# Optimization experiments

Hardware: AMD Instinct MI355X
Metric: run time of the kernel (lower is better)

Reference implementation:

```python
import jax, jax.numpy as jnp
import numpy as np

B, S_VIT, S_Q, L = 64, 257, 32, 512
IMG, HID, C = 1408, 768, 30000
H_CLUB, H_MINE = 32, 64


def setup_inputs() -> dict:
    key = jax.random.key(0)
    ks = jax.random.split(key, 20)
    s = 0.02
    inp = {
        "vit": jax.random.normal(ks[0], (B, S_VIT, IMG), jnp.float32),
        "qformer": jax.random.normal(ks[1], (B, S_Q, HID), jnp.float32),
        "label_pre": jax.random.randint(ks[2], (B, L), 0, C, jnp.int32),
        "perm_idx": jax.random.permutation(ks[3], B).astype(jnp.int32),
        "rand_idx": jax.random.randint(ks[4], (B,), 0, B, jnp.int32),
        # CLUB params
        "W_mu1": jax.random.normal(ks[5], (HID, H_CLUB), jnp.float32) * s,
        "b_mu1": jnp.zeros((H_CLUB,), jnp.float32),
        "W_mu2": jax.random.normal(ks[6], (H_CLUB, C), jnp.float32) * s,
        "b_mu2": jnp.zeros((C,), jnp.float32),
        "W_lv1": jax.random.normal(ks[7], (HID, H_CLUB), jnp.float32) * s,
        "b_lv1": jnp.zeros((H_CLUB,), jnp.float32),
        "W_lv2": jax.random.normal(ks[8], (H_CLUB, C), jnp.float32) * s,
        "b_lv2": jnp.zeros((C,), jnp.float32),
        # MINE params
        "W_t1": jax.random.normal(ks[9], (IMG + HID, H_MINE), jnp.float32) * s,
        "b_t1": jnp.zeros((H_MINE,), jnp.float32),
        "W_t2": jax.random.normal(ks[10], (H_MINE, 1), jnp.float32) * s,
        "b_t2": jnp.zeros((1,), jnp.float32),
    }
    return inp


def reference(vit, qformer, label_pre, perm_idx, rand_idx,
              W_mu1, b_mu1, W_mu2, b_mu2, W_lv1, b_lv1, W_lv2, b_lv2,
              W_t1, b_t1, W_t2, b_t2):
    # label histogram == one_hot(label, C).mean(dim=1), computed via scatter-add
    label = jnp.where(label_pre == -100, 0, label_pre)  # (B, L)
    flat = (label + jnp.arange(B, dtype=label.dtype)[:, None] * C).ravel()
    y_hist = (jnp.zeros((B * C,), jnp.float32).at[flat].add(1.0)
              .reshape(B, C) / jnp.float32(L))  # (B, C)

    xq = qformer.mean(axis=1)  # (B, HID)

    # CLUBSample.forward(xq, y_hist)
    mu = jax.nn.relu(xq @ W_mu1 + b_mu1) @ W_mu2 + b_mu2          # (B, C)
    logvar = jnp.tanh(jax.nn.relu(xq @ W_lv1 + b_lv1) @ W_lv2 + b_lv2)
    inv_var = 1.0 / (jnp.exp(logvar) + 1e-6)
    pos = -(mu - y_hist) ** 2 * inv_var
    neg = -(mu - y_hist[perm_idx]) ** 2 * inv_var
    I_zy = (pos.sum(axis=-1) - neg.sum(axis=-1)).mean() / 2.0

    # MINE.forward(xv, xq)
    xv = vit.mean(axis=1)  # (B, IMG)

    def T(a, b):
        h = jnp.concatenate([a, b], axis=-1)
        return (jax.nn.relu(h @ W_t1 + b_t1) @ W_t2 + b_t2)[:, 0]

    T0 = T(xv, xq)
    T1 = T(xv, xq[rand_idx])
    I_xz = T0.mean() - (jax.nn.logsumexp(T1) - jnp.log(jnp.float32(B)))

    return I_zy - 0.1 * I_xz
```

## Files before the change

kernel.cpp:

```cpp
#include <hip/hip_runtime.h>
#include <hip/hip_bf16.h>
#include <math.h>

#define B       64
#define S_VIT   257
#define S_Q     32
#define L       512
#define IMG     1408
#define HID     768
#define C       30000
#define H_CLUB  32
#define H_MINE  64

#define OFF_XVSUM   0
#define OFF_YHIST   (OFF_XVSUM + B * IMG)
#define OFF_DV64    (OFF_YHIST + B * C)
#define OFF_DQ64    (OFF_DV64 + 2 * B * H_MINE)
#define WS_ZERO_FLOATS (OFF_DQ64 + 2 * B * H_MINE)
#define OFF_XQ      WS_ZERO_FLOATS
#define OFF_HMU     (OFF_XQ + B * HID)
#define OFF_HLV     (OFF_HMU + B * H_CLUB)
#define OFF_CLUBP   (OFF_HLV + B * H_CLUB)
#define N_CLUB_BLK_X 118
#define N_CLUB_BLK_Y 4
#define N_CLUB_PART (N_CLUB_BLK_X * N_CLUB_BLK_Y)

__global__ void k_stage_a(const float* __restrict__ vit, const float* __restrict__ qf,
                          const int* __restrict__ label,
                          float* __restrict__ xv_sum, float* __restrict__ xq,
                          float* __restrict__ y_hist) {
    const int blk = blockIdx.x;
    const int tid = threadIdx.x;
    if (blk < 512) {
        const int b     = blk >> 3;
        const int split = blk & 7;
        const int s0 = split * 33;
        const int s1 = (s0 + 33 < S_VIT) ? s0 + 33 : S_VIT;
        const float4* row = (const float4*)(vit + (size_t)b * S_VIT * IMG);
        float4 a0 = make_float4(0.f, 0.f, 0.f, 0.f);
        float4 a1 = make_float4(0.f, 0.f, 0.f, 0.f);
        const bool second = (tid < 96);
        for (int s = s0; s < s1; ++s) {
            const float4* p = row + (size_t)s * (IMG / 4);
            float4 v = p[tid];
            a0.x += v.x; a0.y += v.y; a0.z += v.z; a0.w += v.w;
            if (second) {
                float4 w = p[tid + 256];
                a1.x += w.x; a1.y += w.y; a1.z += w.z; a1.w += w.w;
            }
        }
        float* out = xv_sum + (size_t)b * IMG;
        atomicAdd(&out[tid * 4 + 0], a0.x);
        atomicAdd(&out[tid * 4 + 1], a0.y);
        atomicAdd(&out[tid * 4 + 2], a0.z);
        atomicAdd(&out[tid * 4 + 3], a0.w);
        if (second) {
            atomicAdd(&out[(tid + 256) * 4 + 0], a1.x);
            atomicAdd(&out[(tid + 256) * 4 + 1], a1.y);
            atomicAdd(&out[(tid + 256) * 4 + 2], a1.z);
            atomicAdd(&out[(tid + 256) * 4 + 3], a1.w);
        }
    } else if (blk < 560) {
        const int idx = (blk - 512) * 256 + tid;
        const int b  = idx / (HID / 4);
        const int k4 = idx % (HID / 4);
        const float* base = qf + (size_t)b * S_Q * HID + k4 * 4;
        float4 s = make_float4(0.f, 0.f, 0.f, 0.f);
        #pragma unroll
        for (int t = 0; t < S_Q; ++t) {
            const float4 v = *(const float4*)(base + (size_t)t * HID);
            s.x += v.x; s.y += v.y; s.z += v.z; s.w += v.w;
        }
        const float inv = 1.0f / (float)S_Q;
        s.x *= inv; s.y *= inv; s.z *= inv; s.w *= inv;
        ((float4*)xq)[(size_t)b * (HID / 4) + k4] = s;
    } else {
        const int idx = (blk - 560) * 256 + tid;
        for (int t = idx; t < B * L; t += 2048) {
            int lab = label[t];
            if (lab == -100) lab = 0;
            const int b = t >> 9;
            atomicAdd(&y_hist[(size_t)b * C + lab], 1.0f);
        }
    }
}

__global__ void __launch_bounds__(256, 2)
k_stage_b(const float* __restrict__ xv_sum, const float* __restrict__ xq,
          const float* __restrict__ W_t1,
          const float* __restrict__ W_mu1, const float* __restrict__ b_mu1,
          const float* __restrict__ W_lv1, const float* __restrict__ b_lv1,
          double* __restrict__ dv, double* __restrict__ dq,
          float* __restrict__ h_mu, float* __restrict__ h_lv) {
    const int blk = blockIdx.x;
    const int tid = threadIdx.x;
    if (blk < 256) {
        __shared__ double s_v[4][H_MINE];
        __shared__ double s_q[4][H_MINE];
        const int b  = blk >> 2;
        const int q  = blk & 3;
        const int j  = tid & 63;
        const int kk = tid >> 6;
        const float* xvb = xv_sum + (size_t)b * IMG;
        const float* xqb = xq + (size_t)b * HID;

        double a0 = 0, a1 = 0, a2 = 0, a3 = 0;
        {
            const int k0 = q * (IMG / 4) + kk * (IMG / 16);
            #pragma unroll 2
            for (int t = 0; t < IMG / 16; t += 4) {
                const int k = k0 + t;
                a0 = fma((double)xvb[k],     (double)W_t1[(size_t)(k)     * H_MINE + j], a0);
                a1 = fma((double)xvb[k + 1], (double)W_t1[(size_t)(k + 1) * H_MINE + j], a1);
                a2 = fma((double)xvb[k + 2], (double)W_t1[(size_t)(k + 2) * H_MINE + j], a2);
                a3 = fma((double)xvb[k + 3], (double)W_t1[(size_t)(k + 3) * H_MINE + j], a3);
            }
        }
        s_v[kk][j] = (a0 + a1) + (a2 + a3);

        double q0 = 0, q1 = 0, q2 = 0, q3 = 0;
        {
            const int k0 = q * (HID / 4) + kk * (HID / 16);
            #pragma unroll 2
            for (int t = 0; t < HID / 16; t += 4) {
                const int k = k0 + t;
                q0 = fma((double)xqb[k],     (double)W_t1[(size_t)(IMG + k)     * H_MINE + j], q0);
                q1 = fma((double)xqb[k + 1], (double)W_t1[(size_t)(IMG + k + 1) * H_MINE + j], q1);
                q2 = fma((double)xqb[k + 2], (double)W_t1[(size_t)(IMG + k + 2) * H_MINE + j], q2);
                q3 = fma((double)xqb[k + 3], (double)W_t1[(size_t)(IMG + k + 3) * H_MINE + j], q3);
            }
        }
        s_q[kk][j] = (q0 + q1) + (q2 + q3);
        __syncthreads();
        if (tid < H_MINE) {
            double sv = (s_v[0][tid] + s_v[1][tid]) + (s_v[2][tid] + s_v[3][tid]);
            double sq = (s_q[0][tid] + s_q[1][tid]) + (s_q[2][tid] + s_q[3][tid]);
            atomicAdd(&dv[b * H_MINE + tid], sv * (1.0 / (double)S_VIT));
            atomicAdd(&dq[b * H_MINE + tid], sq);
        }
    } else {
        __shared__ float  sx[HID];
        __shared__ double s_mu[32][H_CLUB];
        __shared__ double s_lv[32][H_CLUB];
        const int b = blk - 256;
        for (int i = tid; i < HID; i += 256) sx[i] = xq[(size_t)b * HID + i];
        __syncthreads();
        const int h4 = (tid & 7) * 4;
        const int kk = tid >> 3;
        const int k0 = kk * 24;
        double m0 = 0, m1 = 0, m2 = 0, m3 = 0;
        double l0 = 0, l1 = 0, l2 = 0, l3 = 0;
        #pragma unroll 4
        for (int t = 0; t < 24; ++t) {
            const int k = k0 + t;
            const float4 wm = *(const float4*)&W_mu1[(size_t)k * H_CLUB + h4];
            const float4 wl = *(const float4*)&W_lv1[(size_t)k * H_CLUB + h4];
            const double xv = (double)sx[k];
            m0 = fma(xv, (double)wm.x, m0);
            m1 = fma(xv, (double)wm.y, m1);
            m2 = fma(xv, (double)wm.z, m2);
            m3 = fma(xv, (double)wm.w, m3);
            l0 = fma(xv, (double)wl.x, l0);
            l1 = fma(xv, (double)wl.y, l1);
            l2 = fma(xv, (double)wl.z, l2);
            l3 = fma(xv, (double)wl.w, l3);
        }
        s_mu[kk][h4 + 0] = m0; s_mu[kk][h4 + 1] = m1;
        s_mu[kk][h4 + 2] = m2; s_mu[kk][h4 + 3] = m3;
        s_lv[kk][h4 + 0] = l0; s_lv[kk][h4 + 1] = l1;
        s_lv[kk][h4 + 2] = l2; s_lv[kk][h4 + 3] = l3;
        __syncthreads();
        if (tid < H_CLUB) {
            double am = (double)b_mu1[tid], al = (double)b_lv1[tid];
            #pragma unroll
            for (int i = 0; i < 32; ++i) { am += s_mu[i][tid]; al += s_lv[i][tid]; }
            h_mu[b * H_CLUB + tid] = fmaxf((float)am, 0.f);
            h_lv[b * H_CLUB + tid] = fmaxf((float)al, 0.f);
        }
    }
}

__global__ void k_club_main(const float* __restrict__ W_mu2, const float* __restrict__ b_mu2,
                            const float* __restrict__ W_lv2, const float* __restrict__ b_lv2,
                            const float* __restrict__ h_mu, const float* __restrict__ h_lv,
                            const float* __restrict__ y_hist, const int* __restrict__ perm,
                            double* __restrict__ club_partial) {
    __shared__ float s_hmu[16 * H_CLUB];
    __shared__ float s_hlv[16 * H_CLUB];
    __shared__ int   s_perm[16];
    __shared__ double red[256];
    const int tid = threadIdx.x;
    const int c   = blockIdx.x * 256 + tid;
    const int b0  = blockIdx.y * 16;
    if (tid < 16) s_perm[tid] = perm[b0 + tid];
    for (int i = tid; i < 16 * H_CLUB; i += 256) {
        s_hmu[i] = h_mu[b0 * H_CLUB + i];
        s_hlv[i] = h_lv[b0 * H_CLUB + i];
    }
    __syncthreads();

    double total = 0.0;
    if (c < C) {
        float wm[H_CLUB], wl[H_CLUB];
        #pragma unroll
        for (int h = 0; h < H_CLUB; ++h) {
            wm[h] = W_mu2[(size_t)h * C + c];
            wl[h] = W_lv2[(size_t)h * C + c];
        }
        const float bm = b_mu2[c], bl = b_lv2[c];
        for (int bb = 0; bb < 16; ++bb) {
            float mu = bm, lv = bl;
            #pragma unroll
            for (int h = 0; h < H_CLUB; ++h) {
                mu = fmaf(s_hmu[bb * H_CLUB + h], wm[h], mu);
                lv = fmaf(s_hlv[bb * H_CLUB + h], wl[h], lv);
            }
            const float th = tanhf(lv);
            const float iv = 1.0f / (expf(th) + 1e-6f);
            const int b = b0 + bb;
            const float y  = y_hist[(size_t)b * C + c] * (1.0f / (float)L);
            const float yp = y_hist[(size_t)s_perm[bb] * C + c] * (1.0f / (float)L);
            const float dn = mu - yp;
            const float dp = mu - y;
            total += (double)(iv * (dn * dn - dp * dp));
        }
    }
    red[tid] = total;
    __syncthreads();
    for (int off = 128; off > 0; off >>= 1) {
        if (tid < off) red[tid] += red[tid + off];
        __syncthreads();
    }
    if (tid == 0) club_partial[blockIdx.y * gridDim.x + blockIdx.x] = red[0];
}

__global__ void k_final(const double* __restrict__ dv, const double* __restrict__ dq,
                        const float* __restrict__ b_t1, const float* __restrict__ W_t2,
                        const float* __restrict__ b_t2, const int* __restrict__ rand_idx,
                        const double* __restrict__ club_partial,
                        float* __restrict__ out) {
    __shared__ double red[256];
    const int tid = threadIdx.x;
    double cp = 0.0;
    for (int i = tid; i < N_CLUB_PART; i += 256) cp += club_partial[i];
    red[tid] = cp;
    __syncthreads();
    for (int off = 128; off > 0; off >>= 1) {
        if (tid < off) red[tid] += red[tid + off];
        __syncthreads();
    }
    const double club_total = red[0];

    if (tid < B) {
        const int b  = tid;
        const int rb = rand_idx[b];
        double a0 = 0.0, a1 = 0.0;
        #pragma unroll 4
        for (int j = 0; j < H_MINE; ++j) {
            const double base_v = dv[b * H_MINE + j] + (double)b_t1[j];
            const double v0 = base_v + dq[b * H_MINE + j];
            const double v1 = base_v + dq[rb * H_MINE + j];
            const double w = (double)W_t2[j];
            a0 = fma(fmax(v0, 0.0), w, a0);
            a1 = fma(fmax(v1, 0.0), w, a1);
        }
        const double T0 = a0 + (double)b_t2[0];
        const double T1 = a1 + (double)b_t2[0];

        double msum = T0;
        #pragma unroll
        for (int off = 32; off > 0; off >>= 1) msum += __shfl_down(msum, off, 64);
        double mx = T1;
        #pragma unroll
        for (int off = 32; off > 0; off >>= 1) mx = fmax(mx, __shfl_down(mx, off, 64));
        mx = __shfl(mx, 0, 64);
        double e = exp(T1 - mx);
        #pragma unroll
        for (int off = 32; off > 0; off >>= 1) e += __shfl_down(e, off, 64);

        if (tid == 0) {
            const double mean0 = msum * (1.0 / (double)B);
            const double lse   = mx + log(e);
            const double I_xz  = mean0 - (lse - log((double)B));
            const double I_zy  = club_total / (2.0 * (double)B);
            out[0] = (float)(I_zy - 0.1 * I_xz);
        }
    }
}

extern "C" void kernel_launch(void* const* d_in, const int* in_sizes, int n_in,
                              void* d_out, int out_size, void* d_ws, size_t ws_size,
                              hipStream_t stream) {
    const float* vit     = (const float*)d_in[0];
    const float* qformer = (const float*)d_in[1];
    const int*   label   = (const int*)d_in[2];
    const int*   perm    = (const int*)d_in[3];
    const int*   randi   = (const int*)d_in[4];
    const float* W_mu1   = (const float*)d_in[5];
    const float* b_mu1   = (const float*)d_in[6];
    const float* W_mu2   = (const float*)d_in[7];
    const float* b_mu2   = (const float*)d_in[8];
    const float* W_lv1   = (const float*)d_in[9];
    const float* b_lv1   = (const float*)d_in[10];
    const float* W_lv2   = (const float*)d_in[11];
    const float* b_lv2   = (const float*)d_in[12];
    const float* W_t1    = (const float*)d_in[13];
    const float* b_t1    = (const float*)d_in[14];
    const float* W_t2    = (const float*)d_in[15];
    const float* b_t2    = (const float*)d_in[16];

    float* ws      = (float*)d_ws;
    float* xv_sum  = ws + OFF_XVSUM;
    float* y_hist  = ws + OFF_YHIST;
    double* dv64   = (double*)(ws + OFF_DV64);
    double* dq64   = (double*)(ws + OFF_DQ64);
    float* xq      = ws + OFF_XQ;
    float* h_mu    = ws + OFF_HMU;
    float* h_lv    = ws + OFF_HLV;
    double* club_p = (double*)(ws + OFF_CLUBP);

    hipMemsetAsync(ws, 0, (size_t)WS_ZERO_FLOATS * sizeof(float), stream);

    k_stage_a<<<568, 256, 0, stream>>>(vit, qformer, label, xv_sum, xq, y_hist);
    k_stage_b<<<320, 256, 0, stream>>>(xv_sum, xq, W_t1, W_mu1, b_mu1, W_lv1, b_lv1,
                                       dv64, dq64, h_mu, h_lv);
    k_club_main<<<dim3(N_CLUB_BLK_X, N_CLUB_BLK_Y), 256, 0, stream>>>(
        W_mu2, b_mu2, W_lv2, b_lv2, h_mu, h_lv, y_hist, perm, club_p);
    k_final<<<1, 256, 0, stream>>>(dv64, dq64, b_t1, W_t2, b_t2, randi, club_p, (float*)d_out);
}
```

Baseline: 220.9 us.

## Fuse final reduction into CLUB kernel via last-block atomic ticket

Merges the single-block final kernel into the CLUB main kernel. Each block writes its partial, takes an atomic ticket on a zeroed counter, and the last block to finish does the cross-block reduction plus the MINE tail. The CLUB inner loop also reads the hidden vectors from shared memory as float4 instead of scalar loads. This removes one kernel launch and its gap at the cost of extra fences and an atomic per block.

Result: slower. 228.8 us (+3.6%).

```diff
diff --git a/kernel.cpp b/kernel.cpp
--- a/kernel.cpp
+++ b/kernel.cpp
@@ -16,7 +16,8 @@
 #define OFF_YHIST   (OFF_XVSUM + B * IMG)
 #define OFF_DV64    (OFF_YHIST + B * C)
 #define OFF_DQ64    (OFF_DV64 + 2 * B * H_MINE)
-#define WS_ZERO_FLOATS (OFF_DQ64 + 2 * B * H_MINE)
+#define OFF_CTR     (OFF_DQ64 + 2 * B * H_MINE)
+#define WS_ZERO_FLOATS (OFF_CTR + 4)
 #define OFF_XQ      WS_ZERO_FLOATS
 #define OFF_HMU     (OFF_XQ + B * HID)
 #define OFF_HLV     (OFF_HMU + B * H_CLUB)
@@ -180,15 +181,21 @@
     }
 }
 
-__global__ void k_club_main(const float* __restrict__ W_mu2, const float* __restrict__ b_mu2,
-                            const float* __restrict__ W_lv2, const float* __restrict__ b_lv2,
-                            const float* __restrict__ h_mu, const float* __restrict__ h_lv,
-                            const float* __restrict__ y_hist, const int* __restrict__ perm,
-                            double* __restrict__ club_partial) {
-    __shared__ float s_hmu[16 * H_CLUB];
-    __shared__ float s_hlv[16 * H_CLUB];
+__global__ void k_club_final(const float* __restrict__ W_mu2, const float* __restrict__ b_mu2,
+                             const float* __restrict__ W_lv2, const float* __restrict__ b_lv2,
+                             const float* __restrict__ h_mu, const float* __restrict__ h_lv,
+                             const float* __restrict__ y_hist, const int* __restrict__ perm,
+                             double* __restrict__ club_partial,
+                             const double* __restrict__ dv, const double* __restrict__ dq,
+                             const float* __restrict__ b_t1, const float* __restrict__ W_t2,
+                             const float* __restrict__ b_t2, const int* __restrict__ rand_idx,
+                             unsigned int* __restrict__ ctr,
+                             float* __restrict__ out) {
+    __shared__ __align__(16) float s_hmu[16 * H_CLUB];
+    __shared__ __align__(16) float s_hlv[16 * H_CLUB];
     __shared__ int   s_perm[16];
     __shared__ double red[256];
+    __shared__ unsigned int s_ticket;
     const int tid = threadIdx.x;
     const int c   = blockIdx.x * 256 + tid;
     const int b0  = blockIdx.y * 16;
@@ -209,11 +216,22 @@
         }
         const float bm = b_mu2[c], bl = b_lv2[c];
         for (int bb = 0; bb < 16; ++bb) {
+            const float4* hm4 = (const float4*)&s_hmu[bb * H_CLUB];
+            const float4* hl4 = (const float4*)&s_hlv[bb * H_CLUB];
             float mu = bm, lv = bl;
             #pragma unroll
-            for (int h = 0; h < H_CLUB; ++h) {
-                mu = fmaf(s_hmu[bb * H_CLUB + h], wm[h], mu);
-                lv = fmaf(s_hlv[bb * H_CLUB + h], wl[h], lv);
+            for (int h8 = 0; h8 < 8; ++h8) {
+                const float4 hm = hm4[h8];
+                const float4 hl = hl4[h8];
+                const int h = h8 * 4;
+                mu = fmaf(hm.x, wm[h + 0], mu);
+                mu = fmaf(hm.y, wm[h + 1], mu);
+                mu = fmaf(hm.z, wm[h + 2], mu);
+                mu = fmaf(hm.w, wm[h + 3], mu);
+                lv = fmaf(hl.x, wl[h + 0], lv);
+                lv = fmaf(hl.y, wl[h + 1], lv);
+                lv = fmaf(hl.z, wl[h + 2], lv);
+                lv = fmaf(hl.w, wl[h + 3], lv);
             }
             const float th = tanhf(lv);
             const float iv = 1.0f / (expf(th) + 1e-6f);
@@ -231,16 +249,15 @@
         if (tid < off) red[tid] += red[tid + off];
         __syncthreads();
     }
-    if (tid == 0) club_partial[blockIdx.y * gridDim.x + blockIdx.x] = red[0];
-}
-
-__global__ void k_final(const double* __restrict__ dv, const double* __restrict__ dq,
-                        const float* __restrict__ b_t1, const float* __restrict__ W_t2,
-                        const float* __restrict__ b_t2, const int* __restrict__ rand_idx,
-                        const double* __restrict__ club_partial,
-                        float* __restrict__ out) {
-    __shared__ double red[256];
-    const int tid = threadIdx.x;
+    if (tid == 0) {
+        club_partial[blockIdx.y * gridDim.x + blockIdx.x] = red[0];
+        __threadfence();
+        s_ticket = atomicAdd(ctr, 1u);
+    }
+    __syncthreads();
+    if (s_ticket != N_CLUB_PART - 1) return;
+    __threadfence();
+
     double cp = 0.0;
     for (int i = tid; i < N_CLUB_PART; i += 256) cp += club_partial[i];
     red[tid] = cp;
@@ -314,6 +331,7 @@
     float* y_hist  = ws + OFF_YHIST;
     double* dv64   = (double*)(ws + OFF_DV64);
     double* dq64   = (double*)(ws + OFF_DQ64);
+    unsigned int* ctr = (unsigned int*)(ws + OFF_CTR);
     float* xq      = ws + OFF_XQ;
     float* h_mu    = ws + OFF_HMU;
     float* h_lv    = ws + OFF_HLV;
@@ -324,7 +342,7 @@
     k_stage_a<<<568, 256, 0, stream>>>(vit, qformer, label, xv_sum, xq, y_hist);
     k_stage_b<<<320, 256, 0, stream>>>(xv_sum, xq, W_t1, W_mu1, b_mu1, W_lv1, b_lv1,
                                        dv64, dq64, h_mu, h_lv);
-    k_club_main<<<dim3(N_CLUB_BLK_X, N_CLUB_BLK_Y), 256, 0, stream>>>(
-        W_mu2, b_mu2, W_lv2, b_lv2, h_mu, h_lv, y_hist, perm, club_p);
-    k_final<<<1, 256, 0, stream>>>(dv64, dq64, b_t1, W_t2, b_t2, randi, club_p, (float*)d_out);
+    k_club_final<<<dim3(N_CLUB_BLK_X, N_CLUB_BLK_Y), 256, 0, stream>>>(
+        W_mu2, b_mu2, W_lv2, b_lv2, h_mu, h_lv, y_hist, perm, club_p,
+        dv64, dq64, b_t1, W_t2, b_t2, randi, ctr, (float*)d_out);
 }
```

## Skip CLUB classes absent from labels and fuse stages with last-block reduction

Applied to the files above, without the earlier changes.

The term (mu-yp)^2-(mu-y)^2 is zero for any class that appears in neither sample b's labels nor its permuted partner's labels. So each batch block now builds a shared-memory hash set of those labels and evaluates mu and logvar only for that sparse set, instead of all 30000 classes for every batch. The CLUB first layer, the sparse CLUB evaluation, the MINE projection and the final reduction are fused into one kernel. A global atomic ticket lets the last block finish the reduction, which removes two launches and the h_mu/h_lv round-trip. The vit mean is also split across 16 blocks per batch instead of 8. The cost is scattered strided reads of W_mu2/W_lv2 columns, hash insertion contention, and larger shared-memory usage per block.

Result: slower. 312.1 us (+41.2%).

```diff
diff --git a/kernel.cpp b/kernel.cpp
--- a/kernel.cpp
+++ b/kernel.cpp
@@ -16,14 +16,12 @@
 #define OFF_YHIST   (OFF_XVSUM + B * IMG)
 #define OFF_DV64    (OFF_YHIST + B * C)
 #define OFF_DQ64    (OFF_DV64 + 2 * B * H_MINE)
-#define WS_ZERO_FLOATS (OFF_DQ64 + 2 * B * H_MINE)
+#define OFF_CTR     (OFF_DQ64 + 2 * B * H_MINE)
+#define WS_ZERO_FLOATS (OFF_CTR + 4)
 #define OFF_XQ      WS_ZERO_FLOATS
-#define OFF_HMU     (OFF_XQ + B * HID)
-#define OFF_HLV     (OFF_HMU + B * H_CLUB)
-#define OFF_CLUBP   (OFF_HLV + B * H_CLUB)
-#define N_CLUB_BLK_X 118
-#define N_CLUB_BLK_Y 4
-#define N_CLUB_PART (N_CLUB_BLK_X * N_CLUB_BLK_Y)
+#define OFF_CLUBP   (OFF_XQ + B * HID)
+
+#define N_BC_BLOCKS (256 + B)
 
 __global__ void k_stage_a(const float* __restrict__ vit, const float* __restrict__ qf,
                           const int* __restrict__ label,
@@ -31,11 +29,11 @@
                           float* __restrict__ y_hist) {
     const int blk = blockIdx.x;
     const int tid = threadIdx.x;
-    if (blk < 512) {
-        const int b     = blk >> 3;
-        const int split = blk & 7;
-        const int s0 = split * 33;
-        const int s1 = (s0 + 33 < S_VIT) ? s0 + 33 : S_VIT;
+    if (blk < 1024) {
+        const int b     = blk >> 4;
+        const int split = blk & 15;
+        const int s0 = (split * S_VIT) >> 4;
+        const int s1 = ((split + 1) * S_VIT) >> 4;
         const float4* row = (const float4*)(vit + (size_t)b * S_VIT * IMG);
         float4 a0 = make_float4(0.f, 0.f, 0.f, 0.f);
         float4 a1 = make_float4(0.f, 0.f, 0.f, 0.f);
@@ -60,8 +58,8 @@
             atomicAdd(&out[(tid + 256) * 4 + 2], a1.z);
             atomicAdd(&out[(tid + 256) * 4 + 3], a1.w);
         }
-    } else if (blk < 560) {
-        const int idx = (blk - 512) * 256 + tid;
+    } else if (blk < 1072) {
+        const int idx = (blk - 1024) * 256 + tid;
         const int b  = idx / (HID / 4);
         const int k4 = idx % (HID / 4);
         const float* base = qf + (size_t)b * S_Q * HID + k4 * 4;
@@ -75,7 +73,7 @@
         s.x *= inv; s.y *= inv; s.z *= inv; s.w *= inv;
         ((float4*)xq)[(size_t)b * (HID / 4) + k4] = s;
     } else {
-        const int idx = (blk - 560) * 256 + tid;
+        const int idx = (blk - 1072) * 256 + tid;
         for (int t = idx; t < B * L; t += 2048) {
             int lab = label[t];
             if (lab == -100) lab = 0;
@@ -86,17 +84,36 @@
 }
 
 __global__ void __launch_bounds__(256, 2)
-k_stage_b(const float* __restrict__ xv_sum, const float* __restrict__ xq,
-          const float* __restrict__ W_t1,
-          const float* __restrict__ W_mu1, const float* __restrict__ b_mu1,
-          const float* __restrict__ W_lv1, const float* __restrict__ b_lv1,
-          double* __restrict__ dv, double* __restrict__ dq,
-          float* __restrict__ h_mu, float* __restrict__ h_lv) {
+k_stage_bc(const float* __restrict__ xv_sum, const float* __restrict__ xq,
+           const float* __restrict__ W_t1,
+           const float* __restrict__ W_mu1, const float* __restrict__ b_mu1,
+           const float* __restrict__ W_lv1, const float* __restrict__ b_lv1,
+           const float* __restrict__ W_mu2, const float* __restrict__ b_mu2,
+           const float* __restrict__ W_lv2, const float* __restrict__ b_lv2,
+           const float* __restrict__ y_hist, const int* __restrict__ label,
+           const int* __restrict__ perm, const int* __restrict__ rand_idx,
+           const float* __restrict__ b_t1, const float* __restrict__ W_t2,
+           const float* __restrict__ b_t2,
+           double* __restrict__ dv, double* __restrict__ dq,
+           double* __restrict__ club_partial, unsigned int* __restrict__ ctr,
+           float* __restrict__ out) {
+    __shared__ double s_v[4][H_MINE];
+    __shared__ double s_q[4][H_MINE];
+    __shared__ float  sx[HID];
+    __shared__ double s_mu[32][H_CLUB];
+    __shared__ double s_lv[32][H_CLUB];
+    __shared__ float  s_hmu[H_CLUB];
+    __shared__ float  s_hlv[H_CLUB];
+    __shared__ int    htab[2048];
+    __shared__ int    s_list[1024];
+    __shared__ int    s_nlist;
+    __shared__ double red[256];
+    __shared__ unsigned int s_ticket;
+
     const int blk = blockIdx.x;
     const int tid = threadIdx.x;
+
     if (blk < 256) {
-        __shared__ double s_v[4][H_MINE];
-        __shared__ double s_q[4][H_MINE];
         const int b  = blk >> 2;
         const int q  = blk & 3;
         const int j  = tid & 63;
@@ -139,110 +156,102 @@
             atomicAdd(&dq[b * H_MINE + tid], sq);
         }
     } else {
-        __shared__ float  sx[HID];
-        __shared__ double s_mu[32][H_CLUB];
-        __shared__ double s_lv[32][H_CLUB];
-        const int b = blk - 256;
+        const int b  = blk - 256;
+        const int pb = perm[b];
         for (int i = tid; i < HID; i += 256) sx[i] = xq[(size_t)b * HID + i];
         __syncthreads();
-        const int h4 = (tid & 7) * 4;
-        const int kk = tid >> 3;
-        const int k0 = kk * 24;
-        double m0 = 0, m1 = 0, m2 = 0, m3 = 0;
-        double l0 = 0, l1 = 0, l2 = 0, l3 = 0;
-        #pragma unroll 4
-        for (int t = 0; t < 24; ++t) {
-            const int k = k0 + t;
-            const float4 wm = *(const float4*)&W_mu1[(size_t)k * H_CLUB + h4];
-            const float4 wl = *(const float4*)&W_lv1[(size_t)k * H_CLUB + h4];
-            const double xv = (double)sx[k];
-            m0 = fma(xv, (double)wm.x, m0);
-            m1 = fma(xv, (double)wm.y, m1);
-            m2 = fma(xv, (double)wm.z, m2);
-            m3 = fma(xv, (double)wm.w, m3);
-            l0 = fma(xv, (double)wl.x, l0);
-            l1 = fma(xv, (double)wl.y, l1);
-            l2 = fma(xv, (double)wl.z, l2);
-            l3 = fma(xv, (double)wl.w, l3);
-        }
-        s_mu[kk][h4 + 0] = m0; s_mu[kk][h4 + 1] = m1;
-        s_mu[kk][h4 + 2] = m2; s_mu[kk][h4 + 3] = m3;
-        s_lv[kk][h4 + 0] = l0; s_lv[kk][h4 + 1] = l1;
-        s_lv[kk][h4 + 2] = l2; s_lv[kk][h4 + 3] = l3;
+        {
+            const int h4 = (tid & 7) * 4;
+            const int kk = tid >> 3;
+            const int k0 = kk * 24;
+            double m0 = 0, m1 = 0, m2 = 0, m3 = 0;
+            double l0 = 0, l1 = 0, l2 = 0, l3 = 0;
+            #pragma unroll 4
+            for (int t = 0; t < 24; ++t) {
+                const int k = k0 + t;
+                const float4 wm = *(const float4*)&W_mu1[(size_t)k * H_CLUB + h4];
+                const float4 wl = *(const float4*)&W_lv1[(size_t)k * H_CLUB + h4];
+                const double xv = (double)sx[k];
+                m0 = fma(xv, (double)wm.x, m0);
+                m1 = fma(xv, (double)wm.y, m1);
+                m2 = fma(xv, (double)wm.z, m2);
+                m3 = fma(xv, (double)wm.w, m3);
+                l0 = fma(xv, (double)wl.x, l0);
+                l1 = fma(xv, (double)wl.y, l1);
+                l2 = fma(xv, (double)wl.z, l2);
+                l3 = fma(xv, (double)wl.w, l3);
+            }
+            s_mu[kk][h4 + 0] = m0; s_mu[kk][h4 + 1] = m1;
+            s_mu[kk][h4 + 2] = m2; s_mu[kk][h4 + 3] = m3;
+            s_lv[kk][h4 + 0] = l0; s_lv[kk][h4 + 1] = l1;
+            s_lv[kk][h4 + 2] = l2; s_lv[kk][h4 + 3] = l3;
+        }
+        for (int i = tid; i < 2048; i += 256) htab[i] = -1;
+        if (tid == 0) s_nlist = 0;
         __syncthreads();
         if (tid < H_CLUB) {
             double am = (double)b_mu1[tid], al = (double)b_lv1[tid];
             #pragma unroll
             for (int i = 0; i < 32; ++i) { am += s_mu[i][tid]; al += s_lv[i][tid]; }
-            h_mu[b * H_CLUB + tid] = fmaxf((float)am, 0.f);
-            h_lv[b * H_CLUB + tid] = fmaxf((float)al, 0.f);
-        }
-    }
-}
-
-__global__ void k_club_main(const float* __restrict__ W_mu2, const float* __restrict__ b_mu2,
-                            const float* __restrict__ W_lv2, const float* __restrict__ b_lv2,
-                            const float* __restrict__ h_mu, const float* __restrict__ h_lv,
-                            const float* __restrict__ y_hist, const int* __restrict__ perm,
-                            double* __restrict__ club_partial) {
-    __shared__ float s_hmu[16 * H_CLUB];
-    __shared__ float s_hlv[16 * H_CLUB];
-    __shared__ int   s_perm[16];
-    __shared__ double red[256];
-    const int tid = threadIdx.x;
-    const int c   = blockIdx.x * 256 + tid;
-    const int b0  = blockIdx.y * 16;
-    if (tid < 16) s_perm[tid] = perm[b0 + tid];
-    for (int i = tid; i < 16 * H_CLUB; i += 256) {
-        s_hmu[i] = h_mu[b0 * H_CLUB + i];
-        s_hlv[i] = h_lv[b0 * H_CLUB + i];
-    }
-    __syncthreads();
-
-    double total = 0.0;
-    if (c < C) {
-        float wm[H_CLUB], wl[H_CLUB];
-        #pragma unroll
-        for (int h = 0; h < H_CLUB; ++h) {
-            wm[h] = W_mu2[(size_t)h * C + c];
-            wl[h] = W_lv2[(size_t)h * C + c];
-        }
-        const float bm = b_mu2[c], bl = b_lv2[c];
-        for (int bb = 0; bb < 16; ++bb) {
-            float mu = bm, lv = bl;
+            s_hmu[tid] = fmaxf((float)am, 0.f);
+            s_hlv[tid] = fmaxf((float)al, 0.f);
+        }
+        for (int i = tid; i < 2 * L; i += 256) {
+            int raw = (i < L) ? label[(size_t)b * L + i] : label[(size_t)pb * L + (i - L)];
+            int c = (raw == -100) ? 0 : raw;
+            int slot = c & 2047;
+            while (true) {
+                int prev = atomicCAS(&htab[slot], -1, c);
+                if (prev == -1) { int p = atomicAdd(&s_nlist, 1); s_list[p] = c; break; }
+                if (prev == c) break;
+                slot = (slot + 1) & 2047;
+            }
+        }
+        __syncthreads();
+        const int nl = s_nlist;
+        double total = 0.0;
+        for (int i = tid; i < nl; i += 256) {
+            const int c = s_list[i];
+            float wm[H_CLUB], wl[H_CLUB];
             #pragma unroll
             for (int h = 0; h < H_CLUB; ++h) {
-                mu = fmaf(s_hmu[bb * H_CLUB + h], wm[h], mu);
-                lv = fmaf(s_hlv[bb * H_CLUB + h], wl[h], lv);
+                wm[h] = W_mu2[(size_t)h * C + c];
+                wl[h] = W_lv2[(size_t)h * C + c];
+            }
+            float mu = b_mu2[c], lv = b_lv2[c];
+            #pragma unroll
+            for (int h = 0; h < H_CLUB; ++h) {
+                mu = fmaf(s_hmu[h], wm[h], mu);
+                lv = fmaf(s_hlv[h], wl[h], lv);
             }
             const float th = tanhf(lv);
             const float iv = 1.0f / (expf(th) + 1e-6f);
-            const int b = b0 + bb;
-            const float y  = y_hist[(size_t)b * C + c] * (1.0f / (float)L);
-            const float yp = y_hist[(size_t)s_perm[bb] * C + c] * (1.0f / (float)L);
+            const float y  = y_hist[(size_t)b  * C + c] * (1.0f / (float)L);
+            const float yp = y_hist[(size_t)pb * C + c] * (1.0f / (float)L);
             const float dn = mu - yp;
             const float dp = mu - y;
             total += (double)(iv * (dn * dn - dp * dp));
         }
-    }
-    red[tid] = total;
+        red[tid] = total;
+        __syncthreads();
+        for (int off = 128; off > 0; off >>= 1) {
+            if (tid < off) red[tid] += red[tid + off];
+            __syncthreads();
+        }
+        if (tid == 0) club_partial[b] = red[0];
+    }
+
     __syncthreads();
-    for (int off = 128; off > 0; off >>= 1) {
-        if (tid < off) red[tid] += red[tid + off];
-        __syncthreads();
-    }
-    if (tid == 0) club_partial[blockIdx.y * gridDim.x + blockIdx.x] = red[0];
-}
-
-__global__ void k_final(const double* __restrict__ dv, const double* __restrict__ dq,
-                        const float* __restrict__ b_t1, const float* __restrict__ W_t2,
-                        const float* __restrict__ b_t2, const int* __restrict__ rand_idx,
-                        const double* __restrict__ club_partial,
-                        float* __restrict__ out) {
-    __shared__ double red[256];
-    const int tid = threadIdx.x;
+    if (tid == 0) {
+        __threadfence();
+        s_ticket = atomicAdd(ctr, 1u);
+    }
+    __syncthreads();
+    if (s_ticket != N_BC_BLOCKS - 1) return;
+    __threadfence();
+
     double cp = 0.0;
-    for (int i = tid; i < N_CLUB_PART; i += 256) cp += club_partial[i];
+    for (int i = tid; i < B; i += 256) cp += club_partial[i];
     red[tid] = cp;
     __syncthreads();
     for (int off = 128; off > 0; off >>= 1) {
@@ -314,17 +323,15 @@
     float* y_hist  = ws + OFF_YHIST;
     double* dv64   = (double*)(ws + OFF_DV64);
     double* dq64   = (double*)(ws + OFF_DQ64);
+    unsigned int* ctr = (unsigned int*)(ws + OFF_CTR);
     float* xq      = ws + OFF_XQ;
-    float* h_mu    = ws + OFF_HMU;
-    float* h_lv    = ws + OFF_HLV;
     double* club_p = (double*)(ws + OFF_CLUBP);
 
     hipMemsetAsync(ws, 0, (size_t)WS_ZERO_FLOATS * sizeof(float), stream);
 
-    k_stage_a<<<568, 256, 0, stream>>>(vit, qformer, label, xv_sum, xq, y_hist);
-    k_stage_b<<<320, 256, 0, stream>>>(xv_sum, xq, W_t1, W_mu1, b_mu1, W_lv1, b_lv1,
-                                       dv64, dq64, h_mu, h_lv);
-    k_club_main<<<dim3(N_CLUB_BLK_X, N_CLUB_BLK_Y), 256, 0, stream>>>(
-        W_mu2, b_mu2, W_lv2, b_lv2, h_mu, h_lv, y_hist, perm, club_p);
-    k_final<<<1, 256, 0, stream>>>(dv64, dq64, b_t1, W_t2, b_t2, randi, club_p, (float*)d_out);
+    k_stage_a<<<1080, 256, 0, stream>>>(vit, qformer, label, xv_sum, xq, y_hist);
+    k_stage_bc<<<N_BC_BLOCKS, 256, 0, stream>>>(
+        xv_sum, xq, W_t1, W_mu1, b_mu1, W_lv1, b_lv1,
+        W_mu2, b_mu2, W_lv2, b_lv2, y_hist, label, perm, randi,
+        b_t1, W_t2, b_t2, dv64, dq64, club_p, ctr, (float*)d_out);
 }
```
